# Optimization experiments

Measured on AMD Instinct MI355X. Metric: run time of the kernel, lower is better.

The kernel has to match this reference:

```python
import jax, jax.numpy as jnp
import numpy as np
from jax import lax

SD = 16          # sample_duration
STRIDE = 16      # feat_stride
SCALES = (4, 8, 16)
RATIOS = (0.5, 1.0, 2.0)
PRE_NMS = 1000   # proposals kept before NMS (TEST config)
POST_NMS = 128   # proposals kept after NMS
NMS_TH = 0.7


def _anchors2d():
    base = 16.0
    ctr = (base - 1.0) / 2.0
    out = []
    for r in RATIOS:
        ws = np.round(np.sqrt(base * base / r))
        hs = np.round(ws * r)
        for s in SCALES:
            w, h = ws * s, hs * s
            out.append([ctr - (w - 1) / 2, ctr - (h - 1) / 2,
                        ctr + (w - 1) / 2, ctr + (h - 1) / 2])
    return np.asarray(out, np.float32)                       # (9, 4)


def _anchors3d():
    # tube anchors: (x1, y1, t1, x2, y2, t2), durations [SD, SD/2, SD/4]
    a2 = _anchors2d()
    out = []
    for d in (SD, SD // 2, SD // 4):
        for a in a2:
            out.append([a[0], a[1], 0.0, a[2], a[3], d - 1.0])
    return np.asarray(out, np.float32)                       # (27, 6)


def _shifted(anchors, H, W):
    k = anchors.shape[-1]
    sx = jnp.arange(W, dtype=jnp.float32) * STRIDE
    sy = jnp.arange(H, dtype=jnp.float32) * STRIDE
    if k == 4:
        sh = jnp.stack(jnp.broadcast_arrays(sx[None, :], sy[:, None],
                                            sx[None, :], sy[:, None]), -1)
    else:
        z = jnp.zeros((H, W), jnp.float32)
        sh = jnp.stack(jnp.broadcast_arrays(sx[None, :], sy[:, None], z,
                                            sx[None, :], sy[:, None], z), -1)
    return (sh[:, :, None, :] + jnp.asarray(anchors)[None, None]).reshape(-1, k)


def _decode(anchors, deltas):
    # deltas layout: (d_ctr..., d_logsize...); works for 2D (k=4) and 3D (k=6)
    nd = anchors.shape[-1] // 2
    lo, hi = anchors[..., :nd], anchors[..., nd:]
    size = hi - lo + 1.0
    ctr = lo + 0.5 * (size - 1.0)
    pctr = deltas[..., :nd] * size + ctr
    psize = jnp.exp(deltas[..., nd:]) * size
    return jnp.concatenate([pctr - 0.5 * (psize - 1.0),
                            pctr + 0.5 * (psize - 1.0)], -1)


def _iou(b, boxes):
    # b: (k,), boxes: (N, k); area/volume IoU with +1 pixel convention
    nd = boxes.shape[-1] // 2
    lo = jnp.maximum(b[:nd], boxes[:, :nd])
    hi = jnp.minimum(b[nd:], boxes[:, nd:])
    inter = jnp.prod(jnp.maximum(hi - lo + 1.0, 0.0), -1)
    va = jnp.prod(b[nd:] - b[:nd] + 1.0)
    vb = jnp.prod(boxes[:, nd:] - boxes[:, :nd] + 1.0, -1)
    return inter / (va + vb - inter)


def _nms(boxes):
    # boxes already sorted by descending score; greedy NMS, fixed output size
    N = boxes.shape[0]

    def body(i, c):
        supp, keep = c
        idx = jnp.argmax(~supp)                 # first unsuppressed box
        keep = keep.at[i].set(idx.astype(jnp.int32))
        supp = supp | (_iou(boxes[idx], boxes) > NMS_TH)
        supp = supp.at[idx].set(True)
        return supp, keep

    _, keep = lax.fori_loop(0, POST_NMS, body,
                            (jnp.zeros(N, bool), jnp.zeros(POST_NMS, jnp.int32)))
    return keep


def _proposals(scores, deltas, anchors, maxs):
    # scores (B,N), deltas (B,N,k), anchors (N,k), maxs (B,1,k)
    boxes = jnp.clip(_decode(anchors[None], deltas), 0.0, maxs)
    _, idx = lax.top_k(scores, PRE_NMS)
    bx = jnp.take_along_axis(boxes, idx[..., None], axis=1)   # (B,PRE,k)
    keep = jax.vmap(_nms)(bx)                                 # (B,POST)
    sel = jnp.take_along_axis(bx, keep[..., None], axis=1)    # (B,POST,k)
    bidx = jnp.broadcast_to(
        jnp.arange(sel.shape[0], dtype=sel.dtype)[:, None, None],
        sel.shape[:2] + (1,))
    return lax.stop_gradient(jnp.concatenate([bidx, sel], -1))


def setup_inputs() -> dict:
    k = jax.random.split(jax.random.key(0), 8)
    s = 0.01
    return {
        "base_feat": jax.random.normal(k[0], (1, 256, 16, 32, 32), jnp.float32),
        "im_info": jnp.array([[512.0, 512.0, 1.0]], jnp.float32),
        "gt_boxes": jax.random.uniform(k[1], (1, 5, 7), jnp.float32) * 100.0,
        "gt_rois": jax.random.uniform(k[2], (1, 5, 16, 5), jnp.float32) * 100.0,
        "W_conv": jax.random.normal(k[3], (512, 256, 3, 3, 3), jnp.float32) * s,
        "b_conv": jnp.zeros((512,), jnp.float32),
        "W_cls": jax.random.normal(k[4], (54, 512), jnp.float32) * s,
        "b_cls": jnp.zeros((54,), jnp.float32),
        "W_bbox": jax.random.normal(k[5], (162, 512), jnp.float32) * s,
        "b_bbox": jnp.zeros((162,), jnp.float32),
        "W_cls16": jax.random.normal(k[6], (18, 512), jnp.float32) * s,
        "b_cls16": jnp.zeros((18,), jnp.float32),
        "W_bbox16": jax.random.normal(k[7], (36, 512), jnp.float32) * s,
        "b_bbox16": jnp.zeros((36,), jnp.float32),
    }


def reference(base_feat, im_info, gt_boxes, gt_rois, W_conv, b_conv,
              W_cls, b_cls, W_bbox, b_bbox, W_cls16, b_cls16,
              W_bbox16, b_bbox16):
    B, _, T, H, W = base_feat.shape
    # RPN_Conv: 3x3x3 Conv3d + ReLU
    conv1 = jax.nn.relu(
        lax.conv_general_dilated(base_feat, W_conv, (1, 1, 1), "SAME",
                                 dimension_numbers=("NCDHW", "OIDHW", "NCDHW"))
        + b_conv[None, :, None, None, None])
    # 1x1x1 score / bbox heads (3D)
    cls3 = jnp.einsum("bcthw,oc->bothw", conv1, W_cls) + b_cls[None, :, None, None, None]
    bbox3 = jnp.einsum("bcthw,oc->bothw", conv1, W_bbox) + b_bbox[None, :, None, None, None]
    # permute(0,1,3,4,2).mean(4) == mean over the temporal axis
    feat2 = conv1.mean(axis=2)
    cls2 = jnp.einsum("bchw,oc->bohw", feat2, W_cls16) + b_cls16[None, :, None, None]
    bbox2 = jnp.einsum("bchw,oc->bohw", feat2, W_bbox16) + b_bbox16[None, :, None, None]
    # reshape(x,2) + softmax over dim 1; fg prob is the second half of channels
    fg3 = jax.nn.softmax(cls3.reshape(B, 2, 27, T, H, W), axis=1)[:, 1]  # (B,27,T,H,W)
    fg2 = jax.nn.softmax(cls2.reshape(B, 2, 9, H, W), axis=1)[:, 1]      # (B,9,H,W)
    # proposal layers consume detached tensors (torch .data)
    fg3, fg2, bbox3d, bbox2d = map(lax.stop_gradient, (fg3, fg2, bbox3, bbox2))
    # flatten position-major (h, w, anchor)
    sc3 = fg3.mean(axis=2).transpose(0, 2, 3, 1).reshape(B, -1)
    dl3 = bbox3d.mean(axis=2).reshape(B, 27, 6, H, W).transpose(0, 3, 4, 1, 2).reshape(B, -1, 6)
    sc2 = fg2.transpose(0, 2, 3, 1).reshape(B, -1)
    dl2 = bbox2d.reshape(B, 9, 4, H, W).transpose(0, 3, 4, 1, 2).reshape(B, -1, 4)
    imh, imw = im_info[:, 0][:, None], im_info[:, 1][:, None]
    sdm = jnp.full_like(imw, SD - 1.0)
    max3 = jnp.stack([imw - 1, imh - 1, sdm, imw - 1, imh - 1, sdm], -1)  # (B,1,6)
    max2 = jnp.stack([imw - 1, imh - 1, imw - 1, imh - 1], -1)            # (B,1,4)
    rois = _proposals(sc3, dl3, _shifted(_anchors3d(), H, W), max3)       # (B,POST,7)
    rois16 = _proposals(sc2, dl2, _shifted(_anchors2d(), H, W), max2)     # (B,POST,5)
    z = jnp.zeros((), jnp.float32)  # eval mode: all RPN losses are 0
    return rois, rois16, z, z, z, z
```

## Files before the change

### kernel.cpp

```cpp
#include <hip/hip_runtime.h>
#include <hip/hip_bf16.h>
#include <cfloat>
#include <cstdint>


#define T_DIM 16
#define H_DIM 32
#define W_DIM 32
#define NVOX  (T_DIM*H_DIM*W_DIM)
#define HW    (H_DIM*W_DIM)
#define CIN   256
#define COUT  512
#define PRE_NMS 1000
#define POST_NMS 128
#define NMS_TH 0.7f

typedef __attribute__((ext_vector_type(8))) short v8s;
typedef __attribute__((ext_vector_type(4))) float v4f;
typedef __attribute__((ext_vector_type(4))) int v4i;

#define MFMA_B16(A,B,C) __builtin_amdgcn_mfma_f32_16x16x32_bf16(A,B,C,0,0,0)

__device__ __forceinline__ short f2bf(float x) {
    unsigned u = __float_as_uint(x);
    u += 0x7FFFu + ((u >> 16) & 1u);
    return (short)(u >> 16);
}
__device__ __forceinline__ float bf2f(short s) {
    return __uint_as_float(((unsigned)(unsigned short)s) << 16);
}

__constant__ float c_ws[3] = {23.f, 16.f, 11.f};
__constant__ float c_hs[3] = {12.f, 16.f, 22.f};
__constant__ float c_sc[3] = {4.f, 8.f, 16.f};
__constant__ float c_depth[3] = {16.f, 8.f, 4.f};

__global__ void k_split_w(const float* __restrict__ W, short* __restrict__ A0,
                          short* __restrict__ A1, short* __restrict__ A2) {
    int i = blockIdx.x * 256 + threadIdx.x;
    int c7 = i & 7;
    int o = (i >> 3) & 511;
    int ko = (i >> 12) & 31;
    int tap = i >> 17;
    int c = ko * 8 + c7;
    float x = W[(o * 256 + c) * 27 + tap];
    short h = f2bf(x); float r = x - bf2f(h);
    short m = f2bf(r); float r2 = r - bf2f(m);
    short l = f2bf(r2);
    A0[i] = h; A1[i] = m; A2[i] = l;
}

__global__ void k_build_wcomb(const float* __restrict__ Wcls, const float* __restrict__ Wbb,
                              float* __restrict__ Wc) {
    int i = blockIdx.x * 256 + threadIdx.x;
    int o = i & 255;
    int c = i >> 8;
    float v = 0.f;
    if (o < 54) v = Wcls[o * 512 + c];
    else if (o < 216) v = Wbb[(o - 54) * 512 + c];
    Wc[i] = v;
}

#define SPLIT2(X0, X1, OH, OM, OL) {                                          \
    unsigned u0_ = __float_as_uint(X0), u1_ = __float_as_uint(X1);            \
    OH = (int)__builtin_amdgcn_perm(u1_, u0_, 0x07060302u);                   \
    float h0_ = __uint_as_float(u0_ & 0xFFFF0000u);                           \
    float h1_ = __uint_as_float(u1_ & 0xFFFF0000u);                           \
    float r0_ = (X0) - h0_, r1_ = (X1) - h1_;                                 \
    unsigned v0_ = __float_as_uint(r0_), v1_ = __float_as_uint(r1_);          \
    OM = (int)__builtin_amdgcn_perm(v1_, v0_, 0x07060302u);                   \
    float m0_ = __uint_as_float(v0_ & 0xFFFF0000u);                           \
    float m1_ = __uint_as_float(v1_ & 0xFFFF0000u);                           \
    float s0_ = r0_ - m0_, s1_ = r1_ - m1_;                                   \
    OL = (int)__builtin_amdgcn_perm(__float_as_uint(s1_),                     \
                                    __float_as_uint(s0_), 0x07060302u);       \
}

#define CV_SHIFT(TAP) {                                                       \
    int kt_ = (TAP) / 9 - 1, kh_ = ((TAP) / 3) % 3 - 1, kw_ = (TAP) % 3 - 1;  \
    int tt_ = bt + kt_, hh_ = bh + kh_, ww_ = bw + kw_;                       \
    bVal = ((unsigned)tt_ < 16u) && ((unsigned)hh_ < 32u) && ((unsigned)ww_ < 32u); \
    bOff = bVal ? ((tt_ << 10) + (hh_ << 5) + ww_) : 0;                       \
}

#define CV_LOAD_B_RAW(CK) {                                                   \
    const float* ip_ = I + ((size_t)((CK) + skh * 16) << 14) + bOff;          \
    bx0  = bVal ? ip_[0]        : 0.f;                                        \
    bx1  = bVal ? ip_[1 << 14]  : 0.f;                                        \
    bx2  = bVal ? ip_[2 << 14]  : 0.f;                                        \
    bx3  = bVal ? ip_[3 << 14]  : 0.f;                                        \
    bx4  = bVal ? ip_[4 << 14]  : 0.f;                                        \
    bx5  = bVal ? ip_[5 << 14]  : 0.f;                                        \
    bx6  = bVal ? ip_[6 << 14]  : 0.f;                                        \
    bx7  = bVal ? ip_[7 << 14]  : 0.f;                                        \
    bx8  = bVal ? ip_[8 << 14]  : 0.f;                                        \
    bx9  = bVal ? ip_[9 << 14]  : 0.f;                                        \
    bx10 = bVal ? ip_[10 << 14] : 0.f;                                        \
    bx11 = bVal ? ip_[11 << 14] : 0.f;                                        \
    bx12 = bVal ? ip_[12 << 14] : 0.f;                                        \
    bx13 = bVal ? ip_[13 << 14] : 0.f;                                        \
    bx14 = bVal ? ip_[14 << 14] : 0.f;                                        \
    bx15 = bVal ? ip_[15 << 14] : 0.f;                                        \
}

#define CV_SPLIT_B() {                                                        \
    int h01,h23,h45,h67,m01,m23,m45,m67,l01,l23,l45,l67;                      \
    SPLIT2(bx0,  bx1,  h01, m01, l01);                                        \
    SPLIT2(bx2,  bx3,  h23, m23, l23);                                        \
    SPLIT2(bx4,  bx5,  h45, m45, l45);                                        \
    SPLIT2(bx6,  bx7,  h67, m67, l67);                                        \
    pbh0 = (v4i){h01, h23, h45, h67};                                         \
    pbm0 = (v4i){m01, m23, m45, m67};                                         \
    pbl0 = (v4i){l01, l23, l45, l67};                                         \
    SPLIT2(bx8,  bx9,  h01, m01, l01);                                        \
    SPLIT2(bx10, bx11, h23, m23, l23);                                        \
    SPLIT2(bx12, bx13, h45, m45, l45);                                        \
    SPLIT2(bx14, bx15, h67, m67, l67);                                        \
    pbh1 = (v4i){h01, h23, h45, h67};                                         \
    pbm1 = (v4i){m01, m23, m45, m67};                                         \
    pbl1 = (v4i){l01, l23, l45, l67};                                         \
}

#define LOAD_ASET(S) {                                                        \
    const size_t aB_ = (((size_t)((S) >> 3) * 32 + (((S) & 7) << 2)) << 12) + aLane; \
    ah0 = *(const v8s*)(A0 + aB_);       ah1 = *(const v8s*)(A0 + aB_ + 128); \
    ah2 = *(const v8s*)(A0 + aB_ + 256); ah3 = *(const v8s*)(A0 + aB_ + 384); \
    am0 = *(const v8s*)(A1 + aB_);       am1 = *(const v8s*)(A1 + aB_ + 128); \
    am2 = *(const v8s*)(A1 + aB_ + 256); am3 = *(const v8s*)(A1 + aB_ + 384); \
    al0 = *(const v8s*)(A2 + aB_);       al1 = *(const v8s*)(A2 + aB_ + 128); \
    al2 = *(const v8s*)(A2 + aB_ + 256); al3 = *(const v8s*)(A2 + aB_ + 384); \
}

#define COMPUTE() {                                                           \
    _Pragma("unroll")                                                         \
    for (int j = 0; j < 4; ++j) {                                             \
        v8s bb = *(const v8s*)(&Bsh[0][uB + j * 16]);                         \
        v8s bm = *(const v8s*)(&Bsh[1][uB + j * 16]);                         \
        v8s bl = *(const v8s*)(&Bsh[2][uB + j * 16]);                         \
        v4f a;                                                                \
        a = acc[0][j];                                                        \
        a = MFMA_B16(ah0, bb, a); a = MFMA_B16(ah0, bm, a);                   \
        a = MFMA_B16(am0, bb, a); a = MFMA_B16(ah0, bl, a);                   \
        a = MFMA_B16(am0, bm, a); a = MFMA_B16(al0, bb, a);                   \
        acc[0][j] = a;                                                        \
        a = acc[1][j];                                                        \
        a = MFMA_B16(ah1, bb, a); a = MFMA_B16(ah1, bm, a);                   \
        a = MFMA_B16(am1, bb, a); a = MFMA_B16(ah1, bl, a);                   \
        a = MFMA_B16(am1, bm, a); a = MFMA_B16(al1, bb, a);                   \
        acc[1][j] = a;                                                        \
        a = acc[2][j];                                                        \
        a = MFMA_B16(ah2, bb, a); a = MFMA_B16(ah2, bm, a);                   \
        a = MFMA_B16(am2, bb, a); a = MFMA_B16(ah2, bl, a);                   \
        a = MFMA_B16(am2, bm, a); a = MFMA_B16(al2, bb, a);                   \
        acc[2][j] = a;                                                        \
        a = acc[3][j];                                                        \
        a = MFMA_B16(ah3, bb, a); a = MFMA_B16(ah3, bm, a);                   \
        a = MFMA_B16(am3, bb, a); a = MFMA_B16(ah3, bl, a);                   \
        a = MFMA_B16(am3, bm, a); a = MFMA_B16(al3, bb, a);                   \
        acc[3][j] = a;                                                        \
    }                                                                         \
}

__global__ __launch_bounds__(256) void k_conv3d_mfma(
        const float* __restrict__ I, const short* __restrict__ A0,
        const short* __restrict__ A1, const short* __restrict__ A2,
        const float* __restrict__ bias, float* __restrict__ O) {
    __shared__ v4i Bsh[3][512];
    const int tid = threadIdx.x;
    const int o0 = blockIdx.y * 128;
    const int v0 = blockIdx.x * 128;
    const int lane = tid & 63;
    const int wv = tid >> 6;
    const int quad = lane >> 4, m16 = lane & 15;
    const int wo = (wv >> 1) * 64;
    const int wvx = (wv & 1) * 64;

    const int sa_o = tid >> 1, skh = tid & 1;
    const int uW0 = (skh * 2) * 128 + sa_o;
    const int uW1 = (skh * 2 + 1) * 128 + sa_o;

    const int vbase = v0 + sa_o;
    const int bt = vbase >> 10, bh = (vbase >> 5) & 31, bw = vbase & 31;

    const int uB = quad * 128 + wvx + m16;

    const size_t aLane = ((size_t)(o0 + wo + m16) << 3) + ((size_t)quad << 12);

    v4f acc[4][4];
#pragma unroll
    for (int i = 0; i < 4; i++)
#pragma unroll
        for (int j = 0; j < 4; j++) acc[i][j] = (v4f){0.f, 0.f, 0.f, 0.f};

    int bOff, bVal;
    v4i pbh0, pbh1, pbm0, pbm1, pbl0, pbl1;
    v8s ah0, ah1, ah2, ah3, am0, am1, am2, am3, al0, al1, al2, al3;
    float bx0, bx1, bx2, bx3, bx4, bx5, bx6, bx7;
    float bx8, bx9, bx10, bx11, bx12, bx13, bx14, bx15;

    CV_SHIFT(0);
    CV_LOAD_B_RAW(0);
    CV_SPLIT_B();

    for (int s = 0; s < 216; ++s) {
        __syncthreads();
        Bsh[0][uW0] = pbh0; Bsh[0][uW1] = pbh1;
        Bsh[1][uW0] = pbm0; Bsh[1][uW1] = pbm1;
        Bsh[2][uW0] = pbl0; Bsh[2][uW1] = pbl1;
        __syncthreads();
        LOAD_ASET(s);
        {
            int s1 = s + 1;
            if (s1 < 216) {
                if ((s1 & 7) == 0) CV_SHIFT(s1 >> 3);
                CV_LOAD_B_RAW((s1 & 7) << 5);
            }
        }
        COMPUTE();
        if (s + 1 < 216) CV_SPLIT_B();
    }

#pragma unroll
    for (int i = 0; i < 4; ++i) {
#pragma unroll
        for (int r = 0; r < 4; ++r) {
            int o = o0 + wo + i * 16 + quad * 4 + r;
            float bo = bias[o];
            float* dst = O + (size_t)o * NVOX + v0 + wvx + m16;
#pragma unroll
            for (int j = 0; j < 4; ++j)
                dst[j * 16] = fmaxf(acc[i][j][r] + bo, 0.f);
        }
    }
}

__global__ __launch_bounds__(256) void k_gemm_logits3(const float* __restrict__ conv1,
                                                      const float* __restrict__ Wc,
                                                      float* __restrict__ L) {
    __shared__ float As[16][128];
    __shared__ float Bs[16][128];
    const int tid = threadIdx.x;
    const int o0 = blockIdx.y * 128;
    const int v0 = blockIdx.x * 128;
    const int ty = tid >> 4, tx = tid & 15;

    float acc[8][8];
#pragma unroll
    for (int i = 0; i < 8; i++)
#pragma unroll
        for (int j = 0; j < 8; j++) acc[i][j] = 0.f;

    for (int ck = 0; ck < 512; ck += 16) {
        __syncthreads();
#pragma unroll
        for (int r = 0; r < 2; ++r) {
            int f = tid + r * 256;
            int c_l = f >> 5, o4 = (f & 31) << 2;
            *(float4*)(&As[c_l][o4]) = *(const float4*)(Wc + ((size_t)(ck + c_l) << 8) + o0 + o4);
        }
#pragma unroll
        for (int r = 0; r < 2; ++r) {
            int f = tid + r * 256;
            int c_l = f >> 5, v4 = (f & 31) << 2;
            *(float4*)(&Bs[c_l][v4]) = *(const float4*)(conv1 + ((size_t)(ck + c_l) << 14) + v0 + v4);
        }
        __syncthreads();
#pragma unroll
        for (int k = 0; k < 16; ++k) {
            float a[8], b[8];
            *(float4*)(a)     = *(const float4*)(&As[k][ty * 4]);
            *(float4*)(a + 4) = *(const float4*)(&As[k][64 + ty * 4]);
            *(float4*)(b)     = *(const float4*)(&Bs[k][tx * 4]);
            *(float4*)(b + 4) = *(const float4*)(&Bs[k][64 + tx * 4]);
#pragma unroll
            for (int i = 0; i < 8; i++)
#pragma unroll
                for (int j = 0; j < 8; j++)
                    acc[i][j] = fmaf(a[i], b[j], acc[i][j]);
        }
    }
#pragma unroll
    for (int i = 0; i < 8; i++) {
        int orow = (i < 4) ? (ty * 4 + i) : (64 + ty * 4 + (i - 4));
        float* dst = L + (size_t)(o0 + orow) * NVOX + v0;
        *(float4*)(dst + tx * 4)      = *(const float4*)(&acc[i][0]);
        *(float4*)(dst + 64 + tx * 4) = *(const float4*)(&acc[i][4]);
    }
}

__global__ void k_sc3(const float* __restrict__ L, const float* __restrict__ b_cls,
                      float* __restrict__ sc3) {
    int i = blockIdx.x * 256 + threadIdx.x;
    if (i >= 27 * HW) return;
    int a = i >> 10, hw = i & 1023;
    float b0 = b_cls[a], b1 = b_cls[27 + a];
    const float* L0 = L + (size_t)a * NVOX + hw;
    const float* L1 = L + (size_t)(27 + a) * NVOX + hw;
    float s = 0.f;
    for (int t = 0; t < T_DIM; t++) {
        float x0 = L0[t * HW] + b0, x1 = L1[t * HW] + b1;
        float m = fmaxf(x0, x1);
        float e0 = expf(x0 - m), e1 = expf(x1 - m);
        s += e1 / (e0 + e1);
    }
    sc3[hw * 27 + a] = s * (1.f / 16.f);
}

__global__ void k_dl3(const float* __restrict__ L, const float* __restrict__ b_bbox,
                      float* __restrict__ dl3) {
    int i = blockIdx.x * 256 + threadIdx.x;
    if (i >= 162 * HW) return;
    int ch = i >> 10, hw = i & 1023;
    const float* Lr = L + (size_t)(54 + ch) * NVOX + hw;
    float s = 0.f;
    for (int t = 0; t < T_DIM; t++) s += Lr[t * HW];
    s = s * (1.f / 16.f) + b_bbox[ch];
    int a = ch / 6, d = ch - a * 6;
    dl3[((size_t)hw * 27 + a) * 6 + d] = s;
}

__global__ void k_feat2(const float* __restrict__ conv1, float* __restrict__ feat2) {
    int i = blockIdx.x * 256 + threadIdx.x;
    int c = i >> 10, hw = i & 1023;
    const float* src = conv1 + (size_t)c * NVOX + hw;
    float s = 0.f;
    for (int t = 0; t < T_DIM; t++) s += src[t * HW];
    feat2[i] = s * (1.f / 16.f);
}

__global__ void k_gemm2d(const float* __restrict__ feat2, const float* __restrict__ Wcls16,
                         const float* __restrict__ Wbb16, float* __restrict__ L2) {
    int g = blockIdx.x * 256 + threadIdx.x;
    int o = g >> 10, hw = g & 1023;
    const float* wrow = (o < 18) ? (Wcls16 + (size_t)o * 512) : (Wbb16 + (size_t)(o - 18) * 512);
    float s = 0.f;
    for (int c = 0; c < 512; c++) s = fmaf(wrow[c], feat2[(size_t)c * HW + hw], s);
    L2[(size_t)o * HW + hw] = s;
}

__global__ void k_sc2(const float* __restrict__ L2, const float* __restrict__ b_cls16,
                      float* __restrict__ sc2) {
    int i = blockIdx.x * 256 + threadIdx.x;
    if (i >= 9 * HW) return;
    int a = i >> 10, hw = i & 1023;
    float x0 = L2[(size_t)a * HW + hw] + b_cls16[a];
    float x1 = L2[(size_t)(9 + a) * HW + hw] + b_cls16[9 + a];
    float m = fmaxf(x0, x1);
    float e0 = expf(x0 - m), e1 = expf(x1 - m);
    sc2[hw * 9 + a] = e1 / (e0 + e1);
}

__global__ void k_dl2(const float* __restrict__ L2, const float* __restrict__ b_bbox16,
                      float* __restrict__ dl2) {
    int i = blockIdx.x * 256 + threadIdx.x;
    if (i >= 36 * HW) return;
    int ch = i >> 10, hw = i & 1023;
    float v = L2[(size_t)(18 + ch) * HW + hw] + b_bbox16[ch];
    int a = ch >> 2, d = ch & 3;
    dl2[((size_t)hw * 9 + a) * 4 + d] = v;
}

__device__ __forceinline__ unsigned mapf(float f) {
    unsigned u = __float_as_uint(f);
    return (u & 0x80000000u) ? ~u : (u | 0x80000000u);
}

__global__ __launch_bounds__(1024) void k_proposal(const float* __restrict__ im_info,
                                                   const float* __restrict__ sc3,
                                                   const float* __restrict__ dl3,
                                                   const float* __restrict__ sc2,
                                                   const float* __restrict__ dl2,
                                                   float* __restrict__ out) {
    const int branch = blockIdx.x;
    const int tid = threadIdx.x;
    const int A = (branch == 0) ? 27 : 9;
    const int nd = (branch == 0) ? 3 : 2;
    const float* scores = (branch == 0) ? sc3 : sc2;
    const float* deltas = (branch == 0) ? dl3 : dl2;
    const int K = PRE_NMS;
    const int ept = A;
    const int base = tid * ept;

    __shared__ unsigned hist[256];
    __shared__ unsigned long long keys[1024];
    __shared__ float bx[PRE_NMS][6];
    __shared__ int keep[POST_NMS];
    __shared__ unsigned wsum[16];
    __shared__ unsigned long long alive[16];
    __shared__ int sh_b, sh_next, bcast;

    unsigned prefix = 0;
    int rank = K;
    for (int shift = 24; shift >= 0; shift -= 8) {
        if (tid < 256) hist[tid] = 0;
        __syncthreads();
        const unsigned mask_hi = (shift == 24) ? 0u : (0xFFFFFFFFu << (shift + 8));
        for (int j = 0; j < ept; j++) {
            unsigned m = mapf(scores[base + j]);
            if ((m & mask_hi) == prefix)
                atomicAdd(&hist[(m >> shift) & 255], 1u);
        }
        __syncthreads();
        for (int d = 1; d < 256; d <<= 1) {
            unsigned add = 0;
            if (tid < 256 && tid + d < 256) add = hist[tid + d];
            __syncthreads();
            if (tid < 256) hist[tid] += add;
            __syncthreads();
        }
        if (tid < 256) {
            bool win = (hist[tid] >= (unsigned)rank) &&
                       (tid == 255 || hist[tid + 1] < (unsigned)rank);
            if (win) { sh_b = tid; sh_next = (tid == 255) ? 0 : (int)hist[tid + 1]; }
        }
        __syncthreads();
        prefix |= (unsigned)sh_b << shift;
        rank -= sh_next;
        __syncthreads();
    }
    const unsigned tau = prefix;

    int gt_c = 0, eq_c = 0;
    for (int j = 0; j < ept; j++) {
        unsigned m = mapf(scores[base + j]);
        gt_c += (m > tau);
        eq_c += (m == tau);
    }
    unsigned cnt = ((unsigned)gt_c << 16) | (unsigned)eq_c;
    const int lane = tid & 63, wid = tid >> 6;
    unsigned x = cnt;
    for (int d = 1; d < 64; d <<= 1) {
        unsigned y = __shfl_up(x, d);
        if (lane >= d) x += y;
    }
    if (lane == 63) wsum[wid] = x;
    __syncthreads();
    if (wid == 0) {
        unsigned w = (lane < 16) ? wsum[lane] : 0;
        for (int d = 1; d < 16; d <<= 1) {
            unsigned y = __shfl_up(w, d);
            if (lane >= d) w += y;
        }
        if (lane < 16) wsum[lane] = w;
    }
    __syncthreads();
    unsigned excl = x - cnt + (wid ? wsum[wid - 1] : 0);
    const int c1 = (int)(wsum[15] >> 16);
    int gi = (int)(excl >> 16);
    int ei = (int)(excl & 0xFFFFu);
    for (int j = 0; j < ept; j++) {
        int idx = base + j;
        unsigned m = mapf(scores[idx]);
        unsigned long long key = ((unsigned long long)m << 32) |
                                 (unsigned)(0xFFFFFFFFu - (unsigned)idx);
        if (m > tau) {
            keys[gi++] = key;
        } else if (m == tau) {
            if (c1 + ei < K) keys[c1 + ei] = key;
            ei++;
        }
    }
    if (tid < 1024 - K) keys[K + tid] = 0;
    __syncthreads();

    for (int k = 2; k <= 1024; k <<= 1) {
        for (int j = k >> 1; j > 0; j >>= 1) {
            int ixj = tid ^ j;
            if (ixj > tid) {
                unsigned long long a = keys[tid], b = keys[ixj];
                bool sw2 = ((tid & k) == 0) ? (a < b) : (a > b);
                if (sw2) { keys[tid] = b; keys[ixj] = a; }
            }
            __syncthreads();
        }
    }

    const float imh = im_info[0], imw = im_info[1];
    if (tid < K) {
        int n = (int)(0xFFFFFFFFu - (unsigned)(keys[tid] & 0xFFFFFFFFull));
        int cell = n / A, a = n - cell * A;
        int hc = cell >> 5, wc = cell & 31;
        int a2 = (branch == 0) ? (a % 9) : a;
        int ri = a2 / 3, si = a2 % 3;
        float w = c_ws[ri] * c_sc[si], h = c_hs[ri] * c_sc[si];
        float lo[3], hi[3], mx[3];
        lo[0] = 7.5f - (w - 1.f) * 0.5f + 16.f * wc;
        hi[0] = 7.5f + (w - 1.f) * 0.5f + 16.f * wc;
        mx[0] = imw - 1.f;
        lo[1] = 7.5f - (h - 1.f) * 0.5f + 16.f * hc;
        hi[1] = 7.5f + (h - 1.f) * 0.5f + 16.f * hc;
        mx[1] = imh - 1.f;
        if (branch == 0) { lo[2] = 0.f; hi[2] = c_depth[a / 9] - 1.f; mx[2] = (float)(T_DIM - 1); }
        const float* dp = deltas + (size_t)n * (2 * nd);
        for (int d = 0; d < nd; d++) {
            float size = hi[d] - lo[d] + 1.f;
            float ctr = lo[d] + 0.5f * (size - 1.f);
            float pctr = dp[d] * size + ctr;
            float psize = expf(dp[nd + d]) * size;
            float pl = pctr - 0.5f * (psize - 1.f);
            float ph = pctr + 0.5f * (psize - 1.f);
            bx[tid][d]      = fminf(fmaxf(pl, 0.f), mx[d]);
            bx[tid][nd + d] = fminf(fmaxf(ph, 0.f), mx[d]);
        }
    }
    if (tid < 16) alive[tid] = (tid < 15) ? ~0ull : ((1ull << (K - 15 * 64)) - 1);
    __syncthreads();

    float myb[6]; float myvol = 1.f;
    if (tid < K) {
        for (int d = 0; d < 6; d++) myb[d] = bx[tid][d];
        for (int d = 0; d < nd; d++) myvol *= (myb[nd + d] - myb[d] + 1.f);
    }
    for (int i = 0; i < POST_NMS; ++i) {
        if (tid < 64) {
            unsigned long long wvb = (tid < 16) ? alive[tid] : 0ull;
            int cand = wvb ? (tid * 64 + __ffsll(wvb) - 1) : 0x7fffffff;
#pragma unroll
            for (int off = 32; off; off >>= 1)
                cand = min(cand, __shfl_xor(cand, off));
            if (tid == 0) {
                int m = (cand == 0x7fffffff) ? 0 : cand;
                bcast = m; keep[i] = m;
            }
        }
        __syncthreads();
        int sel = bcast;
        bool s = false;
        if (tid < K) {
            float inter = 1.f, selvol = 1.f;
            for (int d = 0; d < nd; d++) {
                float slo = bx[sel][d], shi = bx[sel][nd + d];
                float l = fmaxf(slo, myb[d]);
                float hh = fminf(shi, myb[nd + d]);
                inter *= fmaxf(hh - l + 1.f, 0.f);
                selvol *= (shi - slo + 1.f);
            }
            float iou = inter / (selvol + myvol - inter);
            s = (iou > NMS_TH) || (tid == sel);
        }
        unsigned long long bal = __ballot(s);
        if (lane == 0 && bal) alive[wid] &= ~bal;
        __syncthreads();
    }

    if (tid < POST_NMS) {
        int k = keep[tid];
        if (branch == 0) {
            float* o = out + (size_t)tid * 7;
            o[0] = 0.f;
            for (int d = 0; d < 6; d++) o[1 + d] = bx[k][d];
        } else {
            float* o = out + 128 * 7 + (size_t)tid * 5;
            o[0] = 0.f;
            for (int d = 0; d < 4; d++) o[1 + d] = bx[k][d];
        }
    }
    if (branch == 0 && tid == 0) {
        out[1536] = 0.f; out[1537] = 0.f; out[1538] = 0.f; out[1539] = 0.f;
    }
}

extern "C" void kernel_launch(void* const* d_in, const int* in_sizes, int n_in,
                              void* d_out, int out_size, void* d_ws, size_t ws_size,
                              hipStream_t stream) {
    (void)in_sizes; (void)n_in; (void)out_size; (void)ws_size;
    const float* base_feat = (const float*)d_in[0];
    const float* im_info   = (const float*)d_in[1];
    const float* W_conv    = (const float*)d_in[4];
    const float* b_conv    = (const float*)d_in[5];
    const float* W_cls     = (const float*)d_in[6];
    const float* b_cls     = (const float*)d_in[7];
    const float* W_bbox    = (const float*)d_in[8];
    const float* b_bbox    = (const float*)d_in[9];
    const float* W_cls16   = (const float*)d_in[10];
    const float* b_cls16   = (const float*)d_in[11];
    const float* W_bbox16  = (const float*)d_in[12];
    const float* b_bbox16  = (const float*)d_in[13];
    float* out = (float*)d_out;

    char* ws = (char*)d_ws;
    const size_t AW = (size_t)27 * 512 * 256;
    short* A0 = (short*)ws;
    short* A1 = A0 + AW;
    short* A2 = A1 + AW;
    float* L3 = (float*)ws;
    size_t off = AW * 3 * sizeof(short);
    float* Wcomb  = (float*)(ws + off); off += (size_t)512 * 256 * 4;
    float* conv1  = (float*)(ws + off); off += (size_t)COUT * NVOX * 4;
    float* feat2  = (float*)(ws + off); off += (size_t)512 * HW * 4;
    float* L2     = (float*)(ws + off); off += (size_t)64 * HW * 4;
    float* sc3    = (float*)(ws + off); off += (size_t)27 * HW * 4;
    float* dl3    = (float*)(ws + off); off += (size_t)27 * HW * 6 * 4;
    float* sc2    = (float*)(ws + off); off += (size_t)9 * HW * 4;
    float* dl2    = (float*)(ws + off); off += (size_t)9 * HW * 4 * 4;

    k_split_w<<<13824, 256, 0, stream>>>(W_conv, A0, A1, A2);
    k_build_wcomb<<<512, 256, 0, stream>>>(W_cls, W_bbox, Wcomb);
    {
        dim3 g(NVOX / 128, COUT / 128);
        k_conv3d_mfma<<<g, 256, 0, stream>>>(base_feat, A0, A1, A2, b_conv, conv1);
    }
    {
        dim3 g(NVOX / 128, 2);
        k_gemm_logits3<<<g, 256, 0, stream>>>(conv1, Wcomb, L3);
    }
    k_sc3<<<(27 * HW + 255) / 256, 256, 0, stream>>>(L3, b_cls, sc3);
    k_dl3<<<(162 * HW + 255) / 256, 256, 0, stream>>>(L3, b_bbox, dl3);
    k_feat2<<<(512 * HW) / 256, 256, 0, stream>>>(conv1, feat2);
    k_gemm2d<<<(54 * HW) / 256, 256, 0, stream>>>(feat2, W_cls16, W_bbox16, L2);
    k_sc2<<<(9 * HW + 255) / 256, 256, 0, stream>>>(L2, b_cls16, sc2);
    k_dl2<<<(36 * HW + 255) / 256, 256, 0, stream>>>(L2, b_bbox16, dl2);
    k_proposal<<<2, 1024, 0, stream>>>(im_info, sc3, dl3, sc2, dl2, out);
}
```

Baseline: 973.3 us.

## Load B operands directly into registers per wave, drop LDS staging and barriers

The conv3d MFMA kernel no longer stages the split bf16 input fragments through shared memory with two barriers per K-step. Each lane now loads its own 4x8 input values from global memory, splits them into hi/mid/lo bf16 in registers, and feeds them straight to the MFMAs. This removes LDS traffic and block-wide synchronization. In exchange each wave redundantly loads and splits the B data that the two wave rows previously shared, so global loads and split ALU work double, and register pressure rises.

```diff
diff --git a/kernel.cpp b/kernel.cpp
--- a/kernel.cpp
+++ b/kernel.cpp
@@ -29,6 +29,7 @@
 __device__ __forceinline__ float bf2f(short s) {
     return __uint_as_float(((unsigned)(unsigned short)s) << 16);
 }
+__device__ __forceinline__ v8s asv8s(v4i x) { return __builtin_bit_cast(v8s, x); }
 
 __constant__ float c_ws[3] = {23.f, 16.f, 11.f};
 __constant__ float c_hs[3] = {12.f, 16.f, 22.f};
@@ -76,49 +77,34 @@
                                     __float_as_uint(s0_), 0x07060302u);       \
 }
 
-#define CV_SHIFT(TAP) {                                                       \
+#define CV_SHIFT_J(TAP, J) {                                                  \
     int kt_ = (TAP) / 9 - 1, kh_ = ((TAP) / 3) % 3 - 1, kw_ = (TAP) % 3 - 1;  \
-    int tt_ = bt + kt_, hh_ = bh + kh_, ww_ = bw + kw_;                       \
-    bVal = ((unsigned)tt_ < 16u) && ((unsigned)hh_ < 32u) && ((unsigned)ww_ < 32u); \
-    bOff = bVal ? ((tt_ << 10) + (hh_ << 5) + ww_) : 0;                       \
-}
-
-#define CV_LOAD_B_RAW(CK) {                                                   \
-    const float* ip_ = I + ((size_t)((CK) + skh * 16) << 14) + bOff;          \
-    bx0  = bVal ? ip_[0]        : 0.f;                                        \
-    bx1  = bVal ? ip_[1 << 14]  : 0.f;                                        \
-    bx2  = bVal ? ip_[2 << 14]  : 0.f;                                        \
-    bx3  = bVal ? ip_[3 << 14]  : 0.f;                                        \
-    bx4  = bVal ? ip_[4 << 14]  : 0.f;                                        \
-    bx5  = bVal ? ip_[5 << 14]  : 0.f;                                        \
-    bx6  = bVal ? ip_[6 << 14]  : 0.f;                                        \
-    bx7  = bVal ? ip_[7 << 14]  : 0.f;                                        \
-    bx8  = bVal ? ip_[8 << 14]  : 0.f;                                        \
-    bx9  = bVal ? ip_[9 << 14]  : 0.f;                                        \
-    bx10 = bVal ? ip_[10 << 14] : 0.f;                                        \
-    bx11 = bVal ? ip_[11 << 14] : 0.f;                                        \
-    bx12 = bVal ? ip_[12 << 14] : 0.f;                                        \
-    bx13 = bVal ? ip_[13 << 14] : 0.f;                                        \
-    bx14 = bVal ? ip_[14 << 14] : 0.f;                                        \
-    bx15 = bVal ? ip_[15 << 14] : 0.f;                                        \
-}
-
-#define CV_SPLIT_B() {                                                        \
+    int tt_ = bt##J + kt_, hh_ = bh##J + kh_, ww_ = bw##J + kw_;              \
+    bVal##J = ((unsigned)tt_ < 16u) && ((unsigned)hh_ < 32u) && ((unsigned)ww_ < 32u); \
+    bOff##J = bVal##J ? ((tt_ << 10) + (hh_ << 5) + ww_) : 0;                 \
+}
+
+#define CV_RAW_J(CK, J) {                                                     \
+    const float* p_ = I + ((size_t)((CK) + (quad << 3)) << 14) + bOff##J;     \
+    bx##J##0 = bVal##J ? p_[0]       : 0.f;                                   \
+    bx##J##1 = bVal##J ? p_[1 << 14] : 0.f;                                   \
+    bx##J##2 = bVal##J ? p_[2 << 14] : 0.f;                                   \
+    bx##J##3 = bVal##J ? p_[3 << 14] : 0.f;                                   \
+    bx##J##4 = bVal##J ? p_[4 << 14] : 0.f;                                   \
+    bx##J##5 = bVal##J ? p_[5 << 14] : 0.f;                                   \
+    bx##J##6 = bVal##J ? p_[6 << 14] : 0.f;                                   \
+    bx##J##7 = bVal##J ? p_[7 << 14] : 0.f;                                   \
+}
+
+#define CV_SPLIT_J(J) {                                                       \
     int h01,h23,h45,h67,m01,m23,m45,m67,l01,l23,l45,l67;                      \
-    SPLIT2(bx0,  bx1,  h01, m01, l01);                                        \
-    SPLIT2(bx2,  bx3,  h23, m23, l23);                                        \
-    SPLIT2(bx4,  bx5,  h45, m45, l45);                                        \
-    SPLIT2(bx6,  bx7,  h67, m67, l67);                                        \
-    pbh0 = (v4i){h01, h23, h45, h67};                                         \
-    pbm0 = (v4i){m01, m23, m45, m67};                                         \
-    pbl0 = (v4i){l01, l23, l45, l67};                                         \
-    SPLIT2(bx8,  bx9,  h01, m01, l01);                                        \
-    SPLIT2(bx10, bx11, h23, m23, l23);                                        \
-    SPLIT2(bx12, bx13, h45, m45, l45);                                        \
-    SPLIT2(bx14, bx15, h67, m67, l67);                                        \
-    pbh1 = (v4i){h01, h23, h45, h67};                                         \
-    pbm1 = (v4i){m01, m23, m45, m67};                                         \
-    pbl1 = (v4i){l01, l23, l45, l67};                                         \
+    SPLIT2(bx##J##0, bx##J##1, h01, m01, l01);                                \
+    SPLIT2(bx##J##2, bx##J##3, h23, m23, l23);                                \
+    SPLIT2(bx##J##4, bx##J##5, h45, m45, l45);                                \
+    SPLIT2(bx##J##6, bx##J##7, h67, m67, l67);                                \
+    fh##J = (v4i){h01, h23, h45, h67};                                        \
+    fm##J = (v4i){m01, m23, m45, m67};                                        \
+    fl##J = (v4i){l01, l23, l45, l67};                                        \
 }
 
 #define LOAD_ASET(S) {                                                        \
@@ -131,41 +117,35 @@
     al2 = *(const v8s*)(A2 + aB_ + 256); al3 = *(const v8s*)(A2 + aB_ + 384); \
 }
 
-#define COMPUTE() {                                                           \
-    _Pragma("unroll")                                                         \
-    for (int j = 0; j < 4; ++j) {                                             \
-        v8s bb = *(const v8s*)(&Bsh[0][uB + j * 16]);                         \
-        v8s bm = *(const v8s*)(&Bsh[1][uB + j * 16]);                         \
-        v8s bl = *(const v8s*)(&Bsh[2][uB + j * 16]);                         \
-        v4f a;                                                                \
-        a = acc[0][j];                                                        \
-        a = MFMA_B16(ah0, bb, a); a = MFMA_B16(ah0, bm, a);                   \
-        a = MFMA_B16(am0, bb, a); a = MFMA_B16(ah0, bl, a);                   \
-        a = MFMA_B16(am0, bm, a); a = MFMA_B16(al0, bb, a);                   \
-        acc[0][j] = a;                                                        \
-        a = acc[1][j];                                                        \
-        a = MFMA_B16(ah1, bb, a); a = MFMA_B16(ah1, bm, a);                   \
-        a = MFMA_B16(am1, bb, a); a = MFMA_B16(ah1, bl, a);                   \
-        a = MFMA_B16(am1, bm, a); a = MFMA_B16(al1, bb, a);                   \
-        acc[1][j] = a;                                                        \
-        a = acc[2][j];                                                        \
-        a = MFMA_B16(ah2, bb, a); a = MFMA_B16(ah2, bm, a);                   \
-        a = MFMA_B16(am2, bb, a); a = MFMA_B16(ah2, bl, a);                   \
-        a = MFMA_B16(am2, bm, a); a = MFMA_B16(al2, bb, a);                   \
-        acc[2][j] = a;                                                        \
-        a = acc[3][j];                                                        \
-        a = MFMA_B16(ah3, bb, a); a = MFMA_B16(ah3, bm, a);                   \
-        a = MFMA_B16(am3, bb, a); a = MFMA_B16(ah3, bl, a);                   \
-        a = MFMA_B16(am3, bm, a); a = MFMA_B16(al3, bb, a);                   \
-        acc[3][j] = a;                                                        \
-    }                                                                         \
+#define COMPUTE_J(J, JI) {                                                    \
+    v8s bb = asv8s(fh##J), bm = asv8s(fm##J), bl = asv8s(fl##J);              \
+    v4f a;                                                                    \
+    a = acc[0][JI];                                                           \
+    a = MFMA_B16(ah0, bb, a); a = MFMA_B16(ah0, bm, a);                       \
+    a = MFMA_B16(am0, bb, a); a = MFMA_B16(ah0, bl, a);                       \
+    a = MFMA_B16(am0, bm, a); a = MFMA_B16(al0, bb, a);                       \
+    acc[0][JI] = a;                                                           \
+    a = acc[1][JI];                                                           \
+    a = MFMA_B16(ah1, bb, a); a = MFMA_B16(ah1, bm, a);                       \
+    a = MFMA_B16(am1, bb, a); a = MFMA_B16(ah1, bl, a);                       \
+    a = MFMA_B16(am1, bm, a); a = MFMA_B16(al1, bb, a);                       \
+    acc[1][JI] = a;                                                           \
+    a = acc[2][JI];                                                           \
+    a = MFMA_B16(ah2, bb, a); a = MFMA_B16(ah2, bm, a);                       \
+    a = MFMA_B16(am2, bb, a); a = MFMA_B16(ah2, bl, a);                       \
+    a = MFMA_B16(am2, bm, a); a = MFMA_B16(al2, bb, a);                       \
+    acc[2][JI] = a;                                                           \
+    a = acc[3][JI];                                                           \
+    a = MFMA_B16(ah3, bb, a); a = MFMA_B16(ah3, bm, a);                       \
+    a = MFMA_B16(am3, bb, a); a = MFMA_B16(ah3, bl, a);                       \
+    a = MFMA_B16(am3, bm, a); a = MFMA_B16(al3, bb, a);                       \
+    acc[3][JI] = a;                                                           \
 }
 
 __global__ __launch_bounds__(256) void k_conv3d_mfma(
         const float* __restrict__ I, const short* __restrict__ A0,
         const short* __restrict__ A1, const short* __restrict__ A2,
         const float* __restrict__ bias, float* __restrict__ O) {
-    __shared__ v4i Bsh[3][512];
     const int tid = threadIdx.x;
     const int o0 = blockIdx.y * 128;
     const int v0 = blockIdx.x * 128;
@@ -175,14 +155,14 @@
     const int wo = (wv >> 1) * 64;
     const int wvx = (wv & 1) * 64;
 
-    const int sa_o = tid >> 1, skh = tid & 1;
-    const int uW0 = (skh * 2) * 128 + sa_o;
-    const int uW1 = (skh * 2 + 1) * 128 + sa_o;
-
-    const int vbase = v0 + sa_o;
-    const int bt = vbase >> 10, bh = (vbase >> 5) & 31, bw = vbase & 31;
-
-    const int uB = quad * 128 + wvx + m16;
+    const int vb0 = v0 + wvx + m16;
+    const int bt0 = vb0 >> 10,        bh0 = (vb0 >> 5) & 31,        bw0 = vb0 & 31;
+    const int vb1 = vb0 + 16;
+    const int bt1 = vb1 >> 10,        bh1 = (vb1 >> 5) & 31,        bw1 = vb1 & 31;
+    const int vb2 = vb0 + 32;
+    const int bt2 = vb2 >> 10,        bh2 = (vb2 >> 5) & 31,        bw2 = vb2 & 31;
+    const int vb3 = vb0 + 48;
+    const int bt3 = vb3 >> 10,        bh3 = (vb3 >> 5) & 31,        bw3 = vb3 & 31;
 
     const size_t aLane = ((size_t)(o0 + wo + m16) << 3) + ((size_t)quad << 12);
 
@@ -192,32 +172,41 @@
 #pragma unroll
         for (int j = 0; j < 4; j++) acc[i][j] = (v4f){0.f, 0.f, 0.f, 0.f};
 
-    int bOff, bVal;
-    v4i pbh0, pbh1, pbm0, pbm1, pbl0, pbl1;
+    int bVal0, bVal1, bVal2, bVal3;
+    int bOff0, bOff1, bOff2, bOff3;
+    float bx00, bx01, bx02, bx03, bx04, bx05, bx06, bx07;
+    float bx10, bx11, bx12, bx13, bx14, bx15, bx16, bx17;
+    float bx20, bx21, bx22, bx23, bx24, bx25, bx26, bx27;
+    float bx30, bx31, bx32, bx33, bx34, bx35, bx36, bx37;
+    v4i fh0, fh1, fh2, fh3, fm0, fm1, fm2, fm3, fl0, fl1, fl2, fl3;
     v8s ah0, ah1, ah2, ah3, am0, am1, am2, am3, al0, al1, al2, al3;
-    float bx0, bx1, bx2, bx3, bx4, bx5, bx6, bx7;
-    float bx8, bx9, bx10, bx11, bx12, bx13, bx14, bx15;
-
-    CV_SHIFT(0);
-    CV_LOAD_B_RAW(0);
-    CV_SPLIT_B();
+
+    CV_SHIFT_J(0, 0); CV_SHIFT_J(0, 1); CV_SHIFT_J(0, 2); CV_SHIFT_J(0, 3);
+    CV_RAW_J(0, 0); CV_RAW_J(0, 1); CV_RAW_J(0, 2); CV_RAW_J(0, 3);
+    CV_SPLIT_J(0); CV_SPLIT_J(1); CV_SPLIT_J(2); CV_SPLIT_J(3);
 
     for (int s = 0; s < 216; ++s) {
-        __syncthreads();
-        Bsh[0][uW0] = pbh0; Bsh[0][uW1] = pbh1;
-        Bsh[1][uW0] = pbm0; Bsh[1][uW1] = pbm1;
-        Bsh[2][uW0] = pbl0; Bsh[2][uW1] = pbl1;
-        __syncthreads();
         LOAD_ASET(s);
         {
             int s1 = s + 1;
             if (s1 < 216) {
-                if ((s1 & 7) == 0) CV_SHIFT(s1 >> 3);
-                CV_LOAD_B_RAW((s1 & 7) << 5);
+                if ((s1 & 7) == 0) {
+                    int tap1 = s1 >> 3;
+                    CV_SHIFT_J(tap1, 0); CV_SHIFT_J(tap1, 1);
+                    CV_SHIFT_J(tap1, 2); CV_SHIFT_J(tap1, 3);
+                }
+                int ck1 = (s1 & 7) << 5;
+                CV_RAW_J(ck1, 0); CV_RAW_J(ck1, 1);
+                CV_RAW_J(ck1, 2); CV_RAW_J(ck1, 3);
             }
         }
-        COMPUTE();
-        if (s + 1 < 216) CV_SPLIT_B();
+        COMPUTE_J(0, 0);
+        COMPUTE_J(1, 1);
+        COMPUTE_J(2, 2);
+        COMPUTE_J(3, 3);
+        if (s + 1 < 216) {
+            CV_SPLIT_J(0); CV_SPLIT_J(1); CV_SPLIT_J(2); CV_SPLIT_J(3);
+        }
     }
 
 #pragma unroll
```

After: 1.010 ms. 3.8% more time.

## Pre-split input into padded channel-last bf16 triplets for direct-load conv

Applied to the files above, without the earlier changes.

Adds a pre-pass that transposes the input volume into a zero-padded, channel-last layout and splits each value into three bf16 parts once. The 3D conv kernel then loads B fragments directly from global memory with tap offsets, with no LDS staging, per-tap bounds handling or in-loop splitting. This removes the redundant split work repeated across all 27 taps and all output-channel blocks. The cost is extra workspace, a zeroing pass, a transpose pass, and direct global loads that now depend on cache hit rates. The old LDS path remains as a fallback when the workspace is too small.

```diff
diff --git a/kernel.cpp b/kernel.cpp
--- a/kernel.cpp
+++ b/kernel.cpp
@@ -11,6 +11,7 @@
 #define HW    (H_DIM*W_DIM)
 #define CIN   256
 #define COUT  512
+#define VPAD  (18*34*34)
 #define PRE_NMS 1000
 #define POST_NMS 128
 #define NMS_TH 0.7f
@@ -59,6 +60,152 @@
     if (o < 54) v = Wcls[o * 512 + c];
     else if (o < 216) v = Wbb[(o - 54) * 512 + c];
     Wc[i] = v;
+}
+
+__global__ void k_zero_b(int4* __restrict__ p, int n) {
+    int i = blockIdx.x * 256 + threadIdx.x;
+    if (i < n) p[i] = make_int4(0, 0, 0, 0);
+}
+
+__global__ __launch_bounds__(256) void k_split_i(const float* __restrict__ I,
+                                                 short* __restrict__ BH,
+                                                 short* __restrict__ BM,
+                                                 short* __restrict__ BL) {
+    __shared__ float T[64][65];
+    const int bv = (blockIdx.x & 255) * 64;
+    const int bc = (blockIdx.x >> 8) * 64;
+    const int tx = threadIdx.x & 63, ty = threadIdx.x >> 6;
+#pragma unroll
+    for (int it = 0; it < 16; ++it) {
+        int c_l = ty + it * 4;
+        T[c_l][tx] = I[(size_t)(bc + c_l) * NVOX + bv + tx];
+    }
+    __syncthreads();
+#pragma unroll
+    for (int it = 0; it < 16; ++it) {
+        int vr = ty + it * 4;
+        int v = bv + vr;
+        int t = v >> 10, h = (v >> 5) & 31, w = v & 31;
+        size_t vp = ((size_t)(t + 1) * 34 + (h + 1)) * 34 + (w + 1);
+        float x = T[tx][vr];
+        unsigned u = __float_as_uint(x);
+        float hh = __uint_as_float(u & 0xFFFF0000u);
+        float r = x - hh;
+        unsigned um = __float_as_uint(r);
+        float mm = __uint_as_float(um & 0xFFFF0000u);
+        float l2 = r - mm;
+        size_t o = vp * 256 + bc + tx;
+        BH[o] = (short)(u >> 16);
+        BM[o] = (short)(um >> 16);
+        BL[o] = (short)(__float_as_uint(l2) >> 16);
+    }
+}
+
+#define LOAD_ASET(S) {                                                        \
+    const size_t aB_ = (((size_t)((S) >> 3) * 32 + (((S) & 7) << 2)) << 12) + aLane; \
+    ah0 = *(const v8s*)(A0 + aB_);       ah1 = *(const v8s*)(A0 + aB_ + 128); \
+    ah2 = *(const v8s*)(A0 + aB_ + 256); ah3 = *(const v8s*)(A0 + aB_ + 384); \
+    am0 = *(const v8s*)(A1 + aB_);       am1 = *(const v8s*)(A1 + aB_ + 128); \
+    am2 = *(const v8s*)(A1 + aB_ + 256); am3 = *(const v8s*)(A1 + aB_ + 384); \
+    al0 = *(const v8s*)(A2 + aB_);       al1 = *(const v8s*)(A2 + aB_ + 128); \
+    al2 = *(const v8s*)(A2 + aB_ + 256); al3 = *(const v8s*)(A2 + aB_ + 384); \
+}
+
+#define COMPUTE_FR(FH, FM, FL, JI) {                                          \
+    v4f a;                                                                    \
+    a = acc[0][JI];                                                           \
+    a = MFMA_B16(ah0, FH, a); a = MFMA_B16(ah0, FM, a);                       \
+    a = MFMA_B16(am0, FH, a); a = MFMA_B16(ah0, FL, a);                       \
+    a = MFMA_B16(am0, FM, a); a = MFMA_B16(al0, FH, a);                       \
+    acc[0][JI] = a;                                                           \
+    a = acc[1][JI];                                                           \
+    a = MFMA_B16(ah1, FH, a); a = MFMA_B16(ah1, FM, a);                       \
+    a = MFMA_B16(am1, FH, a); a = MFMA_B16(ah1, FL, a);                       \
+    a = MFMA_B16(am1, FM, a); a = MFMA_B16(al1, FH, a);                       \
+    acc[1][JI] = a;                                                           \
+    a = acc[2][JI];                                                           \
+    a = MFMA_B16(ah2, FH, a); a = MFMA_B16(ah2, FM, a);                       \
+    a = MFMA_B16(am2, FH, a); a = MFMA_B16(ah2, FL, a);                       \
+    a = MFMA_B16(am2, FM, a); a = MFMA_B16(al2, FH, a);                       \
+    acc[2][JI] = a;                                                           \
+    a = acc[3][JI];                                                           \
+    a = MFMA_B16(ah3, FH, a); a = MFMA_B16(ah3, FM, a);                       \
+    a = MFMA_B16(am3, FH, a); a = MFMA_B16(ah3, FL, a);                       \
+    a = MFMA_B16(am3, FM, a); a = MFMA_B16(al3, FH, a);                       \
+    acc[3][JI] = a;                                                           \
+}
+
+__global__ __launch_bounds__(256) void k_conv3d_mfma_ps(
+        const short* __restrict__ BH, const short* __restrict__ BM,
+        const short* __restrict__ BL, const short* __restrict__ A0,
+        const short* __restrict__ A1, const short* __restrict__ A2,
+        const float* __restrict__ bias, float* __restrict__ O) {
+    const int tid = threadIdx.x;
+    const int o0 = blockIdx.y * 128;
+    const int v0 = blockIdx.x * 128;
+    const int lane = tid & 63;
+    const int wv = tid >> 6;
+    const int quad = lane >> 4, m16 = lane & 15;
+    const int wo = (wv >> 1) * 64;
+    const int wvx = (wv & 1) * 64;
+
+    int ib0, ib1, ib2, ib3;
+    {
+        int v = v0 + wvx + m16;
+        int t = v >> 10, h = (v >> 5) & 31, w = v & 31;
+        ib0 = (((t + 1) * 34 + (h + 1)) * 34 + (w + 1)) * 256 + quad * 8;
+        v += 16; t = v >> 10; h = (v >> 5) & 31; w = v & 31;
+        ib1 = (((t + 1) * 34 + (h + 1)) * 34 + (w + 1)) * 256 + quad * 8;
+        v += 16; t = v >> 10; h = (v >> 5) & 31; w = v & 31;
+        ib2 = (((t + 1) * 34 + (h + 1)) * 34 + (w + 1)) * 256 + quad * 8;
+        v += 16; t = v >> 10; h = (v >> 5) & 31; w = v & 31;
+        ib3 = (((t + 1) * 34 + (h + 1)) * 34 + (w + 1)) * 256 + quad * 8;
+    }
+    const size_t aLane = ((size_t)(o0 + wo + m16) << 3) + ((size_t)quad << 12);
+
+    v4f acc[4][4];
+#pragma unroll
+    for (int i = 0; i < 4; i++)
+#pragma unroll
+        for (int j = 0; j < 4; j++) acc[i][j] = (v4f){0.f, 0.f, 0.f, 0.f};
+
+    v8s ah0, ah1, ah2, ah3, am0, am1, am2, am3, al0, al1, al2, al3;
+
+    for (int s = 0; s < 216; ++s) {
+        const int tap = s >> 3;
+        const int kt = tap / 9 - 1, kh = (tap / 3) % 3 - 1, kw = tap % 3 - 1;
+        const int dAdd = (kt * 1156 + kh * 34 + kw) * 256 + ((s & 7) << 5);
+        LOAD_ASET(s);
+        v8s fh0 = *(const v8s*)(BH + (ib0 + dAdd));
+        v8s fm0 = *(const v8s*)(BM + (ib0 + dAdd));
+        v8s fl0 = *(const v8s*)(BL + (ib0 + dAdd));
+        v8s fh1 = *(const v8s*)(BH + (ib1 + dAdd));
+        v8s fm1 = *(const v8s*)(BM + (ib1 + dAdd));
+        v8s fl1 = *(const v8s*)(BL + (ib1 + dAdd));
+        v8s fh2 = *(const v8s*)(BH + (ib2 + dAdd));
+        v8s fm2 = *(const v8s*)(BM + (ib2 + dAdd));
+        v8s fl2 = *(const v8s*)(BL + (ib2 + dAdd));
+        v8s fh3 = *(const v8s*)(BH + (ib3 + dAdd));
+        v8s fm3 = *(const v8s*)(BM + (ib3 + dAdd));
+        v8s fl3 = *(const v8s*)(BL + (ib3 + dAdd));
+        COMPUTE_FR(fh0, fm0, fl0, 0);
+        COMPUTE_FR(fh1, fm1, fl1, 1);
+        COMPUTE_FR(fh2, fm2, fl2, 2);
+        COMPUTE_FR(fh3, fm3, fl3, 3);
+    }
+
+#pragma unroll
+    for (int i = 0; i < 4; ++i) {
+#pragma unroll
+        for (int r = 0; r < 4; ++r) {
+            int o = o0 + wo + i * 16 + quad * 4 + r;
+            float bo = bias[o];
+            float* dst = O + (size_t)o * NVOX + v0 + wvx + m16;
+#pragma unroll
+            for (int j = 0; j < 4; ++j)
+                dst[j * 16] = fmaxf(acc[i][j][r] + bo, 0.f);
+        }
+    }
 }
 
 #define SPLIT2(X0, X1, OH, OM, OL) {                                          \
@@ -121,47 +268,17 @@
     pbl1 = (v4i){l01, l23, l45, l67};                                         \
 }
 
-#define LOAD_ASET(S) {                                                        \
-    const size_t aB_ = (((size_t)((S) >> 3) * 32 + (((S) & 7) << 2)) << 12) + aLane; \
-    ah0 = *(const v8s*)(A0 + aB_);       ah1 = *(const v8s*)(A0 + aB_ + 128); \
-    ah2 = *(const v8s*)(A0 + aB_ + 256); ah3 = *(const v8s*)(A0 + aB_ + 384); \
-    am0 = *(const v8s*)(A1 + aB_);       am1 = *(const v8s*)(A1 + aB_ + 128); \
-    am2 = *(const v8s*)(A1 + aB_ + 256); am3 = *(const v8s*)(A1 + aB_ + 384); \
-    al0 = *(const v8s*)(A2 + aB_);       al1 = *(const v8s*)(A2 + aB_ + 128); \
-    al2 = *(const v8s*)(A2 + aB_ + 256); al3 = *(const v8s*)(A2 + aB_ + 384); \
-}
-
-#define COMPUTE() {                                                           \
+#define COMPUTE_LDS() {                                                       \
     _Pragma("unroll")                                                         \
     for (int j = 0; j < 4; ++j) {                                             \
         v8s bb = *(const v8s*)(&Bsh[0][uB + j * 16]);                         \
         v8s bm = *(const v8s*)(&Bsh[1][uB + j * 16]);                         \
         v8s bl = *(const v8s*)(&Bsh[2][uB + j * 16]);                         \
-        v4f a;                                                                \
-        a = acc[0][j];                                                        \
-        a = MFMA_B16(ah0, bb, a); a = MFMA_B16(ah0, bm, a);                   \
-        a = MFMA_B16(am0, bb, a); a = MFMA_B16(ah0, bl, a);                   \
-        a = MFMA_B16(am0, bm, a); a = MFMA_B16(al0, bb, a);                   \
-        acc[0][j] = a;                                                        \
-        a = acc[1][j];                                                        \
-        a = MFMA_B16(ah1, bb, a); a = MFMA_B16(ah1, bm, a);                   \
-        a = MFMA_B16(am1, bb, a); a = MFMA_B16(ah1, bl, a);                   \
-        a = MFMA_B16(am1, bm, a); a = MFMA_B16(al1, bb, a);                   \
-        acc[1][j] = a;                                                        \
-        a = acc[2][j];                                                        \
-        a = MFMA_B16(ah2, bb, a); a = MFMA_B16(ah2, bm, a);                   \
-        a = MFMA_B16(am2, bb, a); a = MFMA_B16(ah2, bl, a);                   \
-        a = MFMA_B16(am2, bm, a); a = MFMA_B16(al2, bb, a);                   \
-        acc[2][j] = a;                                                        \
-        a = acc[3][j];                                                        \
-        a = MFMA_B16(ah3, bb, a); a = MFMA_B16(ah3, bm, a);                   \
-        a = MFMA_B16(am3, bb, a); a = MFMA_B16(ah3, bl, a);                   \
-        a = MFMA_B16(am3, bm, a); a = MFMA_B16(al3, bb, a);                   \
-        acc[3][j] = a;                                                        \
+        COMPUTE_FR(bb, bm, bl, j);                                            \
     }                                                                         \
 }
 
-__global__ __launch_bounds__(256) void k_conv3d_mfma(
+__global__ __launch_bounds__(256) void k_conv3d_mfma_lds(
         const float* __restrict__ I, const short* __restrict__ A0,
         const short* __restrict__ A1, const short* __restrict__ A2,
         const float* __restrict__ bias, float* __restrict__ O) {
@@ -183,7 +300,6 @@
     const int bt = vbase >> 10, bh = (vbase >> 5) & 31, bw = vbase & 31;
 
     const int uB = quad * 128 + wvx + m16;
-
     const size_t aLane = ((size_t)(o0 + wo + m16) << 3) + ((size_t)quad << 12);
 
     v4f acc[4][4];
@@ -216,7 +332,7 @@
                 CV_LOAD_B_RAW((s1 & 7) << 5);
             }
         }
-        COMPUTE();
+        COMPUTE_LDS();
         if (s + 1 < 216) CV_SPLIT_B();
     }
 
@@ -563,7 +679,7 @@
 extern "C" void kernel_launch(void* const* d_in, const int* in_sizes, int n_in,
                               void* d_out, int out_size, void* d_ws, size_t ws_size,
                               hipStream_t stream) {
-    (void)in_sizes; (void)n_in; (void)out_size; (void)ws_size;
+    (void)in_sizes; (void)n_in; (void)out_size;
     const float* base_feat = (const float*)d_in[0];
     const float* im_info   = (const float*)d_in[1];
     const float* W_conv    = (const float*)d_in[4];
@@ -580,6 +696,7 @@
 
     char* ws = (char*)d_ws;
     const size_t AW = (size_t)27 * 512 * 256;
+    const size_t BW = (size_t)VPAD * 256;
     short* A0 = (short*)ws;
     short* A1 = A0 + AW;
     short* A2 = A1 + AW;
@@ -587,18 +704,31 @@
     size_t off = AW * 3 * sizeof(short);
     float* Wcomb  = (float*)(ws + off); off += (size_t)512 * 256 * 4;
     float* conv1  = (float*)(ws + off); off += (size_t)COUT * NVOX * 4;
-    float* feat2  = (float*)(ws + off); off += (size_t)512 * HW * 4;
-    float* L2     = (float*)(ws + off); off += (size_t)64 * HW * 4;
-    float* sc3    = (float*)(ws + off); off += (size_t)27 * HW * 4;
-    float* dl3    = (float*)(ws + off); off += (size_t)27 * HW * 6 * 4;
-    float* sc2    = (float*)(ws + off); off += (size_t)9 * HW * 4;
-    float* dl2    = (float*)(ws + off); off += (size_t)9 * HW * 4 * 4;
+    const size_t off3 = off;
+    short* BH = (short*)(ws + off3);
+    short* BM = BH + BW;
+    short* BL = BM + BW;
+    char* tail = ws + off3;
+    float* feat2 = (float*)tail; tail += (size_t)512 * HW * 4;
+    float* L2    = (float*)tail; tail += (size_t)64 * HW * 4;
+    float* sc3   = (float*)tail; tail += (size_t)27 * HW * 4;
+    float* dl3   = (float*)tail; tail += (size_t)27 * HW * 6 * 4;
+    float* sc2   = (float*)tail; tail += (size_t)9 * HW * 4;
+    float* dl2   = (float*)tail; tail += (size_t)9 * HW * 4 * 4;
+
+    const bool big = ws_size >= (off3 + BW * 3 * sizeof(short) + (1u << 20));
 
     k_split_w<<<13824, 256, 0, stream>>>(W_conv, A0, A1, A2);
     k_build_wcomb<<<512, 256, 0, stream>>>(W_cls, W_bbox, Wcomb);
-    {
+    if (big) {
+        const int nz = (int)(BW * 3 * sizeof(short) / 16);
+        k_zero_b<<<(nz + 255) / 256, 256, 0, stream>>>((int4*)BH, nz);
+        k_split_i<<<1024, 256, 0, stream>>>(base_feat, BH, BM, BL);
         dim3 g(NVOX / 128, COUT / 128);
-        k_conv3d_mfma<<<g, 256, 0, stream>>>(base_feat, A0, A1, A2, b_conv, conv1);
+        k_conv3d_mfma_ps<<<g, 256, 0, stream>>>(BH, BM, BL, A0, A1, A2, b_conv, conv1);
+    } else {
+        dim3 g(NVOX / 128, COUT / 128);
+        k_conv3d_mfma_lds<<<g, 256, 0, stream>>>(base_feat, A0, A1, A2, b_conv, conv1);
     }
     {
         dim3 g(NVOX / 128, 2);
```

Result: slower. 1.159 ms (+19.1%).
